# Kernel tuning notes

Hardware: AMD Instinct MI355X
Metric: run time of the kernel (lower is better)

Reference implementation:

```python
import jax, jax.numpy as jnp
import numpy as np

N, E, C_IN = 100000, 800000, 128


def setup_inputs() -> dict:
    key = jax.random.key(0)
    ks = jax.random.split(key, 16)
    x = jax.random.normal(ks[0], (N, C_IN), dtype=jnp.float32)
    edge_index = jax.random.randint(ks[1], (2, E), 0, N, dtype=jnp.int64)

    def glorot(k, shape):
        lim = float(np.sqrt(6.0 / (shape[0] + shape[1])))
        return jax.random.uniform(k, shape, jnp.float32, -lim, lim)

    # channels = [128, 128, 256, 256, 256, 112]; layers 0,3 are l_GCN, layers 1,2,4 are l_SAGE
    params = dict(
        alpha=0.1 * jax.random.normal(ks[2], (5,), jnp.float32),  # ReZero alphas (init'd !=0 to exercise path)
        W0=glorot(ks[3], (128, 128)), b0=jnp.zeros((128,), jnp.float32),
        W1=glorot(ks[4], (128, 256)), R1=glorot(ks[5], (128, 256)), b1=jnp.zeros((256,), jnp.float32),
        W2=glorot(ks[6], (256, 256)), R2=glorot(ks[7], (256, 256)), b2=jnp.zeros((256,), jnp.float32),
        W3=glorot(ks[8], (256, 256)), b3=jnp.zeros((256,), jnp.float32),
        W4=glorot(ks[9], (256, 112)), R4=glorot(ks[10], (256, 112)), b4=jnp.zeros((112,), jnp.float32),
    )
    return dict(x=x, edge_index=edge_index, **params)


def reference(x, edge_index, alpha, W0, b0, W1, R1, b1, W2, R2, b2, W3, b3, W4, R4, b4):
    n = x.shape[0]
    row, col = edge_index[0], edge_index[1]
    ones = jnp.ones((row.shape[0],), x.dtype)
    deg = jax.ops.segment_sum(ones, row, num_segments=n)        # out-degree per node
    dinv = jnp.where(deg > 0, jax.lax.rsqrt(jnp.maximum(deg, 1e-12)), 0.0)
    cnt = jnp.maximum(deg, 1.0)[:, None]                        # mean-aggregation denominator

    def gcn_agg(h):  # D^-1/2 A D^-1/2 @ h
        m = h[col] * dinv[col][:, None]                          # [E, C] gather + scale
        return jax.ops.segment_sum(m, row, num_segments=n) * dinv[:, None]

    def mean_agg(h):  # SparseTensor.matmul(h, reduce='mean')
        return jax.ops.segment_sum(h[col], row, num_segments=n) / cnt

    # layer 0: l_GCN, re_list, rezero=1 -> residual from y[0]; dropout = identity (eval)
    t0 = gcn_agg(x) @ W0 + b0
    h = x + alpha[0] * t0
    # layer 1: l_SAGE + relu
    h = jax.nn.relu(mean_agg(h) @ W1 + h @ R1 + b1)
    # layer 2: l_SAGE + relu
    h = jax.nn.relu(mean_agg(h) @ W2 + h @ R2 + b2)
    # layer 3: l_GCN, re_list, rezero=1 -> residual from y[3] (current h)
    t3 = gcn_agg(h) @ W3 + b3
    h = h + alpha[3] * t3
    # layer 4: l_SAGE, no relu, no residual
    h = mean_agg(h) @ W4 + h @ R4 + b4
    return h
```

## Files before the change

kernel.cpp:

```cpp
#include <hip/hip_runtime.h>


typedef __attribute__((ext_vector_type(8))) short bf16x8;
typedef __attribute__((ext_vector_type(4))) float f32x4;

__device__ __forceinline__ float bf2f(unsigned short u) {
    union { unsigned int i; float f; } v; v.i = ((unsigned int)u) << 16; return v.f;
}
__device__ __forceinline__ unsigned short f2bf(float f) {
    union { float f; unsigned int i; } v; v.f = f;
    unsigned int r = (v.i + 0x7fffu + ((v.i >> 16) & 1u)) >> 16;
    return (unsigned short)r;
}


__global__ __launch_bounds__(256) void zero_int_kernel(int* __restrict__ p, int n)
{
    int i = blockIdx.x * 256 + threadIdx.x;
    if (i < n) p[i] = 0;
}

__global__ __launch_bounds__(256) void count_deg_kernel(
    const int* __restrict__ row, int* __restrict__ deg, int E)
{
    int e = blockIdx.x * 256 + threadIdx.x;
    if (e < E) atomicAdd(&deg[row[e]], 1);
}

__global__ __launch_bounds__(1024) void scan_p1_kernel(
    const int* __restrict__ deg, int* __restrict__ rp,
    int* __restrict__ bsum, int n)
{
    __shared__ int wsum[16];
    int t = threadIdx.x, lane = t & 63, w = t >> 6;
    int base = blockIdx.x * 2048;
    int carry = 0;
    #pragma unroll
    for (int half = 0; half < 2; ++half) {
        int i = base + half * 1024 + t;
        int xv = (i < n) ? deg[i] : 0;
        int s = xv;
        #pragma unroll
        for (int off = 1; off < 64; off <<= 1) {
            int v = __shfl_up(s, off, 64);
            if (lane >= off) s += v;
        }
        if (lane == 63) wsum[w] = s;
        __syncthreads();
        if (w == 0 && lane < 16) {
            int ws = wsum[lane];
            #pragma unroll
            for (int off = 1; off < 16; off <<= 1) {
                int v = __shfl_up(ws, off, 64);
                if (lane >= off) ws += v;
            }
            wsum[lane] = ws;
        }
        __syncthreads();
        int wo = (w == 0) ? 0 : wsum[w - 1];
        if (i < n) rp[i + 1] = carry + wo + s;
        carry += wsum[15];
        if (half == 0) __syncthreads();
    }
    if (t == 0) bsum[blockIdx.x] = carry;
}

__global__ __launch_bounds__(64) void scan_p2_kernel(int* __restrict__ bsum, int B)
{
    int lane = threadIdx.x;
    int v = (lane < B) ? bsum[lane] : 0;
    int s = v;
    #pragma unroll
    for (int off = 1; off < 64; off <<= 1) {
        int u = __shfl_up(s, off, 64);
        if (lane >= off) s += u;
    }
    if (lane < B) bsum[lane] = s - v;
}

__global__ __launch_bounds__(1024) void scan_p3_kernel(
    const int* __restrict__ deg, int* __restrict__ rp,
    int* __restrict__ cursor, const int* __restrict__ bsum,
    float* __restrict__ dinv, float* __restrict__ cinv, int n)
{
    int boff = bsum[blockIdx.x];
    int base = blockIdx.x * 2048;
    #pragma unroll
    for (int half = 0; half < 2; ++half) {
        int i = base + half * 1024 + threadIdx.x;
        if (i < n) {
            int d = deg[i];
            int incl = rp[i + 1] + boff;
            rp[i + 1] = incl;
            cursor[i] = incl - d;
            float df = (float)d;
            dinv[i] = (d > 0) ? rsqrtf(df) : 0.0f;
            cinv[i] = 1.0f / fmaxf(df, 1.0f);
        }
    }
    if (blockIdx.x == 0 && threadIdx.x == 0) rp[0] = 0;
}

__global__ __launch_bounds__(256) void fill_csr_kernel(
    const int* __restrict__ row, const int* __restrict__ col,
    int* __restrict__ cursor, int* __restrict__ colS, int E)
{
    int e = blockIdx.x * 256 + threadIdx.x;
    if (e < E) {
        int p = atomicAdd(&cursor[row[e]], 1);
        colS[p] = col[e];
    }
}


__global__ __launch_bounds__(256) void f32_to_bf16_kernel(
    const float* __restrict__ src, unsigned short* __restrict__ dst, int n4)
{
    int i = blockIdx.x * 256 + threadIdx.x;
    if (i >= n4) return;
    float4 v = ((const float4*)src)[i];
    ushort4 o;
    o.x = f2bf(v.x); o.y = f2bf(v.y); o.z = f2bf(v.z); o.w = f2bf(v.w);
    ((ushort4*)dst)[i] = o;
}

__global__ __launch_bounds__(256) void prep_w_kernel(
    const float* __restrict__ S1, int K1,
    const float* __restrict__ S2, int K2,
    int Nout, int Npad, unsigned short* __restrict__ dst)
{
    int Ktot = K1 + K2;
    int idx = blockIdx.x * 256 + threadIdx.x;
    if (idx >= Npad * Ktot) return;
    int n = idx / Ktot, k = idx - n * Ktot;
    float v = 0.0f;
    if (n < Nout)
        v = (k < K1) ? S1[(size_t)k * Nout + n] : S2[(size_t)(k - K1) * Nout + n];
    dst[idx] = f2bf(v);
}


__device__ __forceinline__ void acc8(float* acc, uint4 u, float s) {
    unsigned int xs[4] = {u.x, u.y, u.z, u.w};
    #pragma unroll
    for (int p = 0; p < 4; ++p) {
        union { unsigned int i; float f; } lo, hi;
        lo.i = xs[p] << 16;
        hi.i = xs[p] & 0xffff0000u;
        acc[2 * p]     += s * lo.f;
        acc[2 * p + 1] += s * hi.f;
    }
}

template <int C, bool HAS_ES>
__global__ __launch_bounds__(256) void agg_bf16_kernel(
    const unsigned short* __restrict__ h, int ldh,
    const int* __restrict__ rp, const int* __restrict__ cols,
    const float* __restrict__ escale, const float* __restrict__ nscale,
    unsigned short* __restrict__ out, int ldo, int n)
{
    constexpr int LPE = (C == 256) ? 32 : 16;
    constexpr int EPG = 64 / LPE;
    constexpr int UNR = 4;
    int node = blockIdx.x * 4 + (threadIdx.x >> 6);
    if (node >= n) return;
    int lane = threadIdx.x & 63;
    int grp = lane / LPE, sub = lane % LPE;
    const unsigned short* hc = h + sub * 8;

    int s = rp[node], e = rp[node + 1];
    float acc[8];
    #pragma unroll
    for (int k = 0; k < 8; ++k) acc[k] = 0.0f;

    for (int i = s; i < e; i += UNR * EPG) {
        int cc[UNR]; float sc[UNR]; uint4 uu[UNR];
        #pragma unroll
        for (int u = 0; u < UNR; ++u) {
            int ii = i + u * EPG + grp;
            bool valid = ii < e;
            int c = valid ? cols[ii] : 0;
            cc[u] = c;
            sc[u] = valid ? (HAS_ES ? escale[c] : 1.0f) : 0.0f;
        }
        #pragma unroll
        for (int u = 0; u < UNR; ++u)
            uu[u] = *(const uint4*)(hc + (size_t)cc[u] * ldh);
        #pragma unroll
        for (int u = 0; u < UNR; ++u)
            acc8(acc, uu[u], sc[u]);
    }

    #pragma unroll
    for (int k = 0; k < 8; ++k) {
        if (EPG == 4) acc[k] += __shfl_xor(acc[k], 16, 64);
        acc[k] += __shfl_xor(acc[k], 32, 64);
    }

    if (grp == 0) {
        float ns = nscale[node];
        uint4 o;
        unsigned int* op = (unsigned int*)&o;
        #pragma unroll
        for (int p = 0; p < 4; ++p) {
            unsigned short a = f2bf(acc[2 * p] * ns);
            unsigned short b = f2bf(acc[2 * p + 1] * ns);
            op[p] = (unsigned int)a | ((unsigned int)b << 16);
        }
        *(uint4*)(out + (size_t)node * ldo + sub * 8) = o;
    }
}


__device__ __forceinline__ void g2l16(const unsigned short* g, unsigned short* l) {
    __builtin_amdgcn_global_load_lds(
        (const __attribute__((address_space(1))) unsigned int*)g,
        (__attribute__((address_space(3))) unsigned int*)l, 16, 0, 0);
}

template <int EPI, bool RES_BF16, bool WF32, bool WB16>
__global__ __launch_bounds__(256) void mfma_gemm_kernel(
    const unsigned short* __restrict__ A1, int K1, int lda1,
    const unsigned short* __restrict__ A2, int K2, int lda2,
    const unsigned short* __restrict__ Bt,
    const float* __restrict__ bias,
    const void* __restrict__ res, int ldres,
    const float* __restrict__ alpha_ptr, int alpha_idx,
    float* __restrict__ outf, unsigned short* __restrict__ outb, int ldo,
    int M, int Nout)
{
    __shared__ unsigned short As[3][128 * 32];
    __shared__ unsigned short Bs[3][128 * 32];
    int t = threadIdx.x;
    int m0 = blockIdx.x * 128, n0 = blockIdx.y * 128;
    int Ktot = K1 + K2;
    int w = t >> 6, lane = t & 63;
    int wm = w & 1, wn = w >> 1;
    int q = lane >> 4, l16 = lane & 15;

    int roff = t >> 2;
    int koff = (((t & 3) ^ ((t >> 2) & 3)) * 8);

    int gmA0 = m0 + roff;       if (gmA0 >= M) gmA0 = M - 1;
    int gmA1 = m0 + 64 + roff;  if (gmA1 >= M) gmA1 = M - 1;
    int gnB0 = n0 + roff;
    int gnB1 = n0 + 64 + roff;

    const size_t a0off = (size_t)gmA0, a1off = (size_t)gmA1;

    f32x4 acc[4][4];
    #pragma unroll
    for (int i = 0; i < 4; ++i)
        #pragma unroll
        for (int j = 0; j < 4; ++j)
            #pragma unroll
            for (int r = 0; r < 4; ++r) acc[i][j][r] = 0.0f;

    const int KC = Ktot >> 5;

    auto issue = [&](int kc, int p) {
        int k0 = kc * 32;
        const unsigned short* Ap; int lda, kk;
        if (k0 < K1) { Ap = A1; lda = lda1; kk = k0; }
        else         { Ap = A2; lda = lda2; kk = k0 - K1; }
        g2l16(Ap + a0off * lda + kk + koff, &As[p][w * 512]);
        g2l16(Ap + a1off * lda + kk + koff, &As[p][2048 + w * 512]);
        g2l16(Bt + (size_t)gnB0 * Ktot + k0 + koff, &Bs[p][w * 512]);
        g2l16(Bt + (size_t)gnB1 * Ktot + k0 + koff, &Bs[p][2048 + w * 512]);
    };

    const int cq = (q ^ (l16 & 3)) * 8;
    const int rbA = (wm * 64 + l16) * 32 + cq;
    const int rbB = (wn * 64 + l16) * 32 + cq;

    issue(0, 0);
    if (KC > 1) issue(1, 1);
    if (KC > 2) issue(2, 2);

    int p = 0;
    for (int kc = 0; kc < KC; ++kc) {
        int rem = KC - 1 - kc;
        if (rem >= 2)      asm volatile("s_waitcnt vmcnt(8)" ::: "memory");
        else if (rem == 1) asm volatile("s_waitcnt vmcnt(4)" ::: "memory");
        else               asm volatile("s_waitcnt vmcnt(0)" ::: "memory");
        __builtin_amdgcn_s_barrier();
        asm volatile("" ::: "memory");

        bf16x8 af[4], bfr[4];
        #pragma unroll
        for (int i = 0; i < 4; ++i)
            af[i] = *(const bf16x8*)&As[p][rbA + i * 16 * 32];
        #pragma unroll
        for (int j = 0; j < 4; ++j)
            bfr[j] = *(const bf16x8*)&Bs[p][rbB + j * 16 * 32];

        asm volatile("s_waitcnt lgkmcnt(0)" ::: "memory");
        __builtin_amdgcn_s_barrier();
        asm volatile("" ::: "memory");
        if (kc + 3 < KC) issue(kc + 3, p);

        __builtin_amdgcn_s_setprio(1);
        #pragma unroll
        for (int i = 0; i < 4; ++i)
            #pragma unroll
            for (int j = 0; j < 4; ++j)
                acc[i][j] = __builtin_amdgcn_mfma_f32_16x16x32_bf16(
                    af[i], bfr[j], acc[i][j], 0, 0, 0);
        __builtin_amdgcn_s_setprio(0);

        p = (p == 2) ? 0 : p + 1;
    }

    float alpha = 0.0f;
    if (EPI == 2) alpha = alpha_ptr[alpha_idx];
    #pragma unroll
    for (int i = 0; i < 4; ++i) {
        #pragma unroll
        for (int j = 0; j < 4; ++j) {
            int n = n0 + wn * 64 + j * 16 + l16;
            if (n >= Nout) continue;
            float bv = bias[n];
            #pragma unroll
            for (int r = 0; r < 4; ++r) {
                int m = m0 + wm * 64 + i * 16 + q * 4 + r;
                if (m >= M) continue;
                float v = acc[i][j][r] + bv;
                if (EPI == 1) v = fmaxf(v, 0.0f);
                if (EPI == 2) {
                    float r0 = RES_BF16
                        ? bf2f(((const unsigned short*)res)[(size_t)m * ldres + n])
                        : ((const float*)res)[(size_t)m * ldres + n];
                    v = r0 + alpha * v;
                }
                if (WF32) outf[(size_t)m * ldo + n] = v;
                if (WB16) outb[(size_t)m * ldo + n] = f2bf(v);
            }
        }
    }
}


extern "C" void kernel_launch(void* const* d_in, const int* in_sizes, int n_in,
                              void* d_out, int out_size, void* d_ws, size_t ws_size,
                              hipStream_t stream)
{
    const float* x      = (const float*)d_in[0];
    const int*   ei     = (const int*)d_in[1];
    const float* alpha  = (const float*)d_in[2];
    const float* W0     = (const float*)d_in[3];
    const float* b0     = (const float*)d_in[4];
    const float* W1     = (const float*)d_in[5];
    const float* R1     = (const float*)d_in[6];
    const float* b1     = (const float*)d_in[7];
    const float* W2     = (const float*)d_in[8];
    const float* R2     = (const float*)d_in[9];
    const float* b2     = (const float*)d_in[10];
    const float* W3     = (const float*)d_in[11];
    const float* b3     = (const float*)d_in[12];
    const float* W4     = (const float*)d_in[13];
    const float* R4     = (const float*)d_in[14];
    const float* b4     = (const float*)d_in[15];

    const int N = in_sizes[0] / 128;
    const int E = in_sizes[1] / 2;
    const int* row = ei;
    const int* col = ei + E;

    size_t off = 0;
    auto alloc = [&](size_t bytes) -> void* {
        void* p = (char*)d_ws + off;
        off += (bytes + 255) & ~(size_t)255;
        return p;
    };
    int*   deg    = (int*)alloc((size_t)N * 4);
    int*   rp     = (int*)alloc((size_t)(N + 1) * 4);
    int*   cursor = (int*)alloc((size_t)N * 4);
    int*   colS   = (int*)alloc((size_t)E * 4);
    int*   bsum   = (int*)alloc((size_t)64 * 4);
    float* dinv   = (float*)alloc((size_t)N * 4);
    float* cinv   = (float*)alloc((size_t)N * 4);
    unsigned short* Wt0 = (unsigned short*)alloc((size_t)128 * 128 * 2);
    unsigned short* Wt1 = (unsigned short*)alloc((size_t)256 * 256 * 2);
    unsigned short* Wt2 = (unsigned short*)alloc((size_t)256 * 512 * 2);
    unsigned short* Wt3 = (unsigned short*)alloc((size_t)256 * 256 * 2);
    unsigned short* Wt4 = (unsigned short*)alloc((size_t)128 * 512 * 2);
    unsigned short* Xb  = (unsigned short*)alloc((size_t)N * 128 * 2);
    unsigned short* Gb  = (unsigned short*)alloc((size_t)N * 256 * 2);
    unsigned short* Pb  = (unsigned short*)alloc((size_t)N * 256 * 2);
    unsigned short* Ab  = (unsigned short*)alloc((size_t)N * 256 * 2);
    unsigned short* Hb  = Xb;
    (void)ws_size;

    const int SB = (N + 2047) / 2048;
    zero_int_kernel<<<(N + 255) / 256, 256, 0, stream>>>(deg, N);
    count_deg_kernel<<<(E + 255) / 256, 256, 0, stream>>>(row, deg, E);
    scan_p1_kernel<<<SB, 1024, 0, stream>>>(deg, rp, bsum, N);
    scan_p2_kernel<<<1, 64, 0, stream>>>(bsum, SB);
    scan_p3_kernel<<<SB, 1024, 0, stream>>>(deg, rp, cursor, bsum, dinv, cinv, N);
    fill_csr_kernel<<<(E + 255) / 256, 256, 0, stream>>>(row, col, cursor, colS, E);

    f32_to_bf16_kernel<<<(N * 32 + 255) / 256, 256, 0, stream>>>(x, Xb, N * 32);
    prep_w_kernel<<<(128 * 128 + 255) / 256, 256, 0, stream>>>(W0, 128, nullptr, 0, 128, 128, Wt0);
    prep_w_kernel<<<(256 * 256 + 255) / 256, 256, 0, stream>>>(W1, 128, R1, 128, 256, 256, Wt1);
    prep_w_kernel<<<(256 * 512 + 255) / 256, 256, 0, stream>>>(W2, 256, R2, 256, 256, 256, Wt2);
    prep_w_kernel<<<(256 * 256 + 255) / 256, 256, 0, stream>>>(W3, 256, nullptr, 0, 256, 256, Wt3);
    prep_w_kernel<<<(128 * 512 + 255) / 256, 256, 0, stream>>>(W4, 256, R4, 256, 112, 128, Wt4);

    dim3 aggGrid((N + 3) / 4);
    dim3 g1((N + 127) / 128, 1), g2((N + 127) / 128, 2);

    agg_bf16_kernel<128, true><<<aggGrid, 256, 0, stream>>>(Xb, 128, rp, colS, dinv, dinv, Ab, 128, N);
    mfma_gemm_kernel<2, false, false, true><<<g1, 256, 0, stream>>>(
        Ab, 128, 128, nullptr, 0, 0, Wt0, b0, x, 128, alpha, 0,
        nullptr, Hb, 128, N, 128);

    agg_bf16_kernel<128, false><<<aggGrid, 256, 0, stream>>>(Hb, 128, rp, colS, nullptr, cinv, Ab, 128, N);
    mfma_gemm_kernel<1, false, false, true><<<g2, 256, 0, stream>>>(
        Ab, 128, 128, Hb, 128, 128, Wt1, b1, nullptr, 0, nullptr, 0,
        nullptr, Gb, 256, N, 256);

    agg_bf16_kernel<256, false><<<aggGrid, 256, 0, stream>>>(Gb, 256, rp, colS, nullptr, cinv, Ab, 256, N);
    mfma_gemm_kernel<1, false, false, true><<<g2, 256, 0, stream>>>(
        Ab, 256, 256, Gb, 256, 256, Wt2, b2, nullptr, 0, nullptr, 0,
        nullptr, Pb, 256, N, 256);

    agg_bf16_kernel<256, true><<<aggGrid, 256, 0, stream>>>(Pb, 256, rp, colS, dinv, dinv, Ab, 256, N);
    mfma_gemm_kernel<2, true, false, true><<<g2, 256, 0, stream>>>(
        Ab, 256, 256, nullptr, 0, 0, Wt3, b3, Pb, 256, alpha, 3,
        nullptr, Gb, 256, N, 256);

    agg_bf16_kernel<256, false><<<aggGrid, 256, 0, stream>>>(Gb, 256, rp, colS, nullptr, cinv, Ab, 256, N);
    mfma_gemm_kernel<0, false, true, false><<<g1, 256, 0, stream>>>(
        Ab, 256, 256, Gb, 256, 256, Wt4, b4, nullptr, 0, nullptr, 0,
        (float*)d_out, nullptr, 112, N, 112);
}
```

Baseline: 766.3 us.

## Use 128x256 GEMM tiles with 512 threads and double-buffered LDS

The MFMA GEMM is templated on output tile width. The 256-wide layers now run one 512-thread block per 128-row stripe instead of two 256-thread blocks, so each A tile is loaded from global memory once rather than twice. The LDS pipeline drops from triple to double buffering to keep shared memory in budget, with vmcnt waits adjusted to the new load count. The shallower prefetch may expose more global-load latency, and the grid has half as many blocks.

```diff
diff --git a/kernel.cpp b/kernel.cpp
--- a/kernel.cpp
+++ b/kernel.cpp
@@ -218,8 +218,8 @@
         (__attribute__((address_space(3))) unsigned int*)l, 16, 0, 0);
 }
 
-template <int EPI, bool RES_BF16, bool WF32, bool WB16>
-__global__ __launch_bounds__(256) void mfma_gemm_kernel(
+template <int BN, int EPI, bool RES_BF16, bool WF32, bool WB16>
+__global__ __launch_bounds__(2 * BN) void mfma_gemm_kernel(
     const unsigned short* __restrict__ A1, int K1, int lda1,
     const unsigned short* __restrict__ A2, int K2, int lda2,
     const unsigned short* __restrict__ Bt,
@@ -229,24 +229,19 @@
     float* __restrict__ outf, unsigned short* __restrict__ outb, int ldo,
     int M, int Nout)
 {
-    __shared__ unsigned short As[3][128 * 32];
-    __shared__ unsigned short Bs[3][128 * 32];
+    constexpr int WAVES = BN / 32;
+    constexpr int AI = 256 / BN;
+    __shared__ unsigned short As[2][128 * 32];
+    __shared__ unsigned short Bs[2][BN * 32];
     int t = threadIdx.x;
-    int m0 = blockIdx.x * 128, n0 = blockIdx.y * 128;
+    int m0 = blockIdx.x * 128, n0 = blockIdx.y * BN;
     int Ktot = K1 + K2;
     int w = t >> 6, lane = t & 63;
     int wm = w & 1, wn = w >> 1;
     int q = lane >> 4, l16 = lane & 15;
 
-    int roff = t >> 2;
-    int koff = (((t & 3) ^ ((t >> 2) & 3)) * 8);
-
-    int gmA0 = m0 + roff;       if (gmA0 >= M) gmA0 = M - 1;
-    int gmA1 = m0 + 64 + roff;  if (gmA1 >= M) gmA1 = M - 1;
-    int gnB0 = n0 + roff;
-    int gnB1 = n0 + 64 + roff;
-
-    const size_t a0off = (size_t)gmA0, a1off = (size_t)gmA1;
+    int koff = (((lane & 3) ^ ((lane >> 2) & 3)) * 8);
+    int rsub = lane >> 2;
 
     f32x4 acc[4][4];
     #pragma unroll
@@ -263,10 +258,18 @@
         const unsigned short* Ap; int lda, kk;
         if (k0 < K1) { Ap = A1; lda = lda1; kk = k0; }
         else         { Ap = A2; lda = lda2; kk = k0 - K1; }
-        g2l16(Ap + a0off * lda + kk + koff, &As[p][w * 512]);
-        g2l16(Ap + a1off * lda + kk + koff, &As[p][2048 + w * 512]);
-        g2l16(Bt + (size_t)gnB0 * Ktot + k0 + koff, &Bs[p][w * 512]);
-        g2l16(Bt + (size_t)gnB1 * Ktot + k0 + koff, &Bs[p][2048 + w * 512]);
+        #pragma unroll
+        for (int a = 0; a < AI; ++a) {
+            int rb = a * 16 * WAVES + w * 16;
+            int gm = m0 + rb + rsub; if (gm >= M) gm = M - 1;
+            g2l16(Ap + (size_t)gm * lda + kk + koff, &As[p][rb * 32]);
+        }
+        #pragma unroll
+        for (int b = 0; b < 2; ++b) {
+            int rb = b * 16 * WAVES + w * 16;
+            int gn = n0 + rb + rsub;
+            g2l16(Bt + (size_t)gn * Ktot + k0 + koff, &Bs[p][rb * 32]);
+        }
     };
 
     const int cq = (q ^ (l16 & 3)) * 8;
@@ -275,14 +278,16 @@
 
     issue(0, 0);
     if (KC > 1) issue(1, 1);
-    if (KC > 2) issue(2, 2);
-
-    int p = 0;
+
     for (int kc = 0; kc < KC; ++kc) {
+        int p = kc & 1;
         int rem = KC - 1 - kc;
-        if (rem >= 2)      asm volatile("s_waitcnt vmcnt(8)" ::: "memory");
-        else if (rem == 1) asm volatile("s_waitcnt vmcnt(4)" ::: "memory");
-        else               asm volatile("s_waitcnt vmcnt(0)" ::: "memory");
+        if (rem >= 1) {
+            if constexpr (AI == 2) asm volatile("s_waitcnt vmcnt(4)" ::: "memory");
+            else                   asm volatile("s_waitcnt vmcnt(3)" ::: "memory");
+        } else {
+            asm volatile("s_waitcnt vmcnt(0)" ::: "memory");
+        }
         __builtin_amdgcn_s_barrier();
         asm volatile("" ::: "memory");
 
@@ -297,7 +302,7 @@
         asm volatile("s_waitcnt lgkmcnt(0)" ::: "memory");
         __builtin_amdgcn_s_barrier();
         asm volatile("" ::: "memory");
-        if (kc + 3 < KC) issue(kc + 3, p);
+        if (kc + 2 < KC) issue(kc + 2, p);
 
         __builtin_amdgcn_s_setprio(1);
         #pragma unroll
@@ -307,8 +312,6 @@
                 acc[i][j] = __builtin_amdgcn_mfma_f32_16x16x32_bf16(
                     af[i], bfr[j], acc[i][j], 0, 0, 0);
         __builtin_amdgcn_s_setprio(0);
-
-        p = (p == 2) ? 0 : p + 1;
     }
 
     float alpha = 0.0f;
@@ -407,30 +410,30 @@
     prep_w_kernel<<<(128 * 512 + 255) / 256, 256, 0, stream>>>(W4, 256, R4, 256, 112, 128, Wt4);
 
     dim3 aggGrid((N + 3) / 4);
-    dim3 g1((N + 127) / 128, 1), g2((N + 127) / 128, 2);
+    dim3 g1((N + 127) / 128, 1);
 
     agg_bf16_kernel<128, true><<<aggGrid, 256, 0, stream>>>(Xb, 128, rp, colS, dinv, dinv, Ab, 128, N);
-    mfma_gemm_kernel<2, false, false, true><<<g1, 256, 0, stream>>>(
+    mfma_gemm_kernel<128, 2, false, false, true><<<g1, 256, 0, stream>>>(
         Ab, 128, 128, nullptr, 0, 0, Wt0, b0, x, 128, alpha, 0,
         nullptr, Hb, 128, N, 128);
 
     agg_bf16_kernel<128, false><<<aggGrid, 256, 0, stream>>>(Hb, 128, rp, colS, nullptr, cinv, Ab, 128, N);
-    mfma_gemm_kernel<1, false, false, true><<<g2, 256, 0, stream>>>(
+    mfma_gemm_kernel<256, 1, false, false, true><<<g1, 512, 0, stream>>>(
         Ab, 128, 128, Hb, 128, 128, Wt1, b1, nullptr, 0, nullptr, 0,
         nullptr, Gb, 256, N, 256);
 
     agg_bf16_kernel<256, false><<<aggGrid, 256, 0, stream>>>(Gb, 256, rp, colS, nullptr, cinv, Ab, 256, N);
-    mfma_gemm_kernel<1, false, false, true><<<g2, 256, 0, stream>>>(
+    mfma_gemm_kernel<256, 1, false, false, true><<<g1, 512, 0, stream>>>(
         Ab, 256, 256, Gb, 256, 256, Wt2, b2, nullptr, 0, nullptr, 0,
         nullptr, Pb, 256, N, 256);
 
     agg_bf16_kernel<256, true><<<aggGrid, 256, 0, stream>>>(Pb, 256, rp, colS, dinv, dinv, Ab, 256, N);
-    mfma_gemm_kernel<2, true, false, true><<<g2, 256, 0, stream>>>(
+    mfma_gemm_kernel<256, 2, true, false, true><<<g1, 512, 0, stream>>>(
         Ab, 256, 256, nullptr, 0, 0, Wt3, b3, Pb, 256, alpha, 3,
         nullptr, Gb, 256, N, 256);
 
     agg_bf16_kernel<256, false><<<aggGrid, 256, 0, stream>>>(Gb, 256, rp, colS, nullptr, cinv, Ab, 256, N);
-    mfma_gemm_kernel<0, false, true, false><<<g1, 256, 0, stream>>>(
+    mfma_gemm_kernel<128, 0, false, true, false><<<g1, 256, 0, stream>>>(
         Ab, 256, 256, Gb, 256, 256, Wt4, b4, nullptr, 0, nullptr, 0,
         (float*)d_out, nullptr, 112, N, 112);
 }
```

Result: faster. 727.3 us (-5.1%).
